# Kernel tuning notes

Measured on AMD Instinct MI355X. Metric: run time of the kernel, lower is better.

## Reference

```python
import jax, jax.numpy as jnp
import numpy as np

B, L, D = 2, 2048, 1024
H = 16
HD = D // H  # 64
WINDOW = 256


def setup_inputs() -> dict:
    key = jax.random.key(0)
    k1, k2, k3 = jax.random.split(key, 3)
    s = 0.02
    return {
        "x": jax.random.normal(k1, (B, L, D), dtype=jnp.float32),
        "w_qkv": jax.random.normal(k2, (D, 3 * D), dtype=jnp.float32) * s,
        "b_qkv": jnp.zeros((3 * D,), dtype=jnp.float32),
        "w_out": jax.random.normal(k3, (D, D), dtype=jnp.float32) * s,
        "b_out": jnp.zeros((D,), dtype=jnp.float32),
    }


def _window_mask(seq_len, window_size, dtype):
    # row i allows cols in [i - w//2, i + w//2] inclusive (symmetric band)
    half = window_size // 2
    i = jnp.arange(seq_len)[:, None]
    j = jnp.arange(seq_len)[None, :]
    allowed = jnp.abs(i - j) <= half
    return jnp.where(allowed, jnp.zeros((), dtype), jnp.asarray(-jnp.inf, dtype))


def reference(x, w_qkv, b_qkv, w_out, b_out):
    b, l, d = x.shape
    qkv = x @ w_qkv + b_qkv                        # [B, L, 3D]
    qkv = qkv.reshape(b, l, 3, H, HD)
    q = jnp.transpose(qkv[:, :, 0], (0, 2, 1, 3))   # [B, H, L, HD]
    k = jnp.transpose(qkv[:, :, 1], (0, 2, 1, 3))
    v = jnp.transpose(qkv[:, :, 2], (0, 2, 1, 3))
    scale = 1.0 / np.sqrt(HD)
    scores = jnp.einsum("bhqd,bhkd->bhqk", q, k) * scale
    scores = scores + _window_mask(l, WINDOW, scores.dtype)[None, None]
    attn = jax.nn.softmax(scores, axis=-1)          # dropout: eval mode (p applied only in training)
    out = jnp.einsum("bhqk,bhkd->bhqd", attn, v)    # [B, H, L, HD]
    out = jnp.transpose(out, (0, 2, 1, 3)).reshape(b, l, d)
    return out @ w_out + b_out
```

## Files before the change

kernel.cpp:

```cpp
#include <hip/hip_runtime.h>
#include <math.h>

#define B_    2
#define L_    2048
#define D_    1024
#define H_    16
#define HD_   64
#define HALF_ 128

typedef __attribute__((ext_vector_type(8))) short short8;
typedef __attribute__((ext_vector_type(4))) float f32x4;

__device__ __forceinline__ unsigned short f2bf(float x) {
  unsigned int u = __float_as_uint(x);
  u = (u + 0x7fffu + ((u >> 16) & 1u)) >> 16;
  return (unsigned short)u;
}

__device__ __forceinline__ void async_cp16(const unsigned short* g, unsigned short* l) {
  __builtin_amdgcn_global_load_lds(
      (const __attribute__((address_space(1))) unsigned int*)g,
      (__attribute__((address_space(3))) unsigned int*)l, 16, 0, 0);
}

__device__ __forceinline__ void tr_round32(const float* __restrict__ in,
                                           unsigned short* __restrict__ hi,
                                           int N, int K, int n0, int k0,
                                           float (*t)[33], int tid) {
  {
    const int kl = tid >> 3, nl = (tid & 7) * 4;
    const float4 v = *(const float4*)&in[(size_t)(k0 + kl) * N + n0 + nl];
    t[kl][nl + 0] = v.x; t[kl][nl + 1] = v.y;
    t[kl][nl + 2] = v.z; t[kl][nl + 3] = v.w;
  }
  __syncthreads();
  {
    const int no = tid >> 3, ko = (tid & 7) * 4;
    ushort4 h;
    h.x = f2bf(t[ko + 0][no]);
    h.y = f2bf(t[ko + 1][no]);
    h.z = f2bf(t[ko + 2][no]);
    h.w = f2bf(t[ko + 3][no]);
    *(ushort4*)&hi[(size_t)(n0 + no) * K + k0 + ko] = h;
  }
}

__global__ __launch_bounds__(256) void prep(const float* __restrict__ x,
                                            unsigned short* __restrict__ x_hi,
                                            const float* __restrict__ w_qkv,
                                            unsigned short* __restrict__ wqkvT,
                                            const float* __restrict__ w_out,
                                            unsigned short* __restrict__ woutT) {
  __shared__ float t[32][33];
  const int bx = blockIdx.x, tid = threadIdx.x;
  if (bx < 4096) {
    const int i = (bx * 256 + tid) * 4;
    const float4 a = *(const float4*)&x[i];
    ushort4 h;
    h.x = f2bf(a.x); h.y = f2bf(a.y); h.z = f2bf(a.z); h.w = f2bf(a.w);
    *(ushort4*)&x_hi[i] = h;
  } else if (bx < 7168) {
    const int tb = bx - 4096;
    tr_round32(w_qkv, wqkvT, 3 * D_, D_, (tb % 96) * 32, (tb / 96) * 32, t, tid);
  } else {
    const int tb = bx - 7168;
    tr_round32(w_out, woutT, D_, D_, (tb % 32) * 32, (tb / 32) * 32, t, tid);
  }
}

__global__ __launch_bounds__(256, 3) void gemm_qkv(
    const unsigned short* __restrict__ Ah,
    const unsigned short* __restrict__ Bh,
    const float* __restrict__ bias,
    unsigned short* __restrict__ q_hi,
    unsigned short* __restrict__ kT,
    unsigned short* __restrict__ vTile,
    int N, int K) {
  __shared__ char smraw[33792];
  const int tid  = threadIdx.x;
  const int wave = tid >> 6, lane = tid & 63;

  const int lin = blockIdx.y * gridDim.x + blockIdx.x;
  const int swz = (lin & 7) * 96 + (lin >> 3);
  const int n0 = (swz % 24) * 128, m0 = (swz / 24) * 128;

  const int wm = (wave >> 1) * 64, wn = (wave & 1) * 64;
  const int quad = lane >> 4, ln16 = lane & 15;

  const bool isA = wave < 2;
  const unsigned short* src = isA ? Ah : Bh;
  const int baserow = isA ? m0 : n0;
  const int instbase = (wave & 1) * 8;
  const int dbase = (isA ? 0 : 16384) + instbase * 1024;
  size_t goff[8];
#pragma unroll
  for (int i = 0; i < 8; ++i) {
    const int r = (instbase + i) * 8 + (lane >> 3);
    const int c = (lane & 7) ^ (r & 7);
    goff[i] = (size_t)(baserow + r) * K + c * 8;
  }

  int offA[4], offB[4];
#pragma unroll
  for (int t = 0; t < 4; ++t) {
    const int r = wm + t * 16 + ln16;
    offA[t] = r * 128 + ((quad ^ (r & 7)) * 16);
    const int rn = wn + t * 16 + ln16;
    offB[t] = 16384 + rn * 128 + ((quad ^ (rn & 7)) * 16);
  }

  f32x4 acc[4][4] = {};
  const char* smb = (const char*)smraw;

  for (int k0 = 0; k0 < K; k0 += 64) {
#pragma unroll
    for (int i = 0; i < 8; ++i)
      async_cp16(src + goff[i] + k0,
                 (unsigned short*)(smraw + dbase + i * 1024));
    __syncthreads();

    {
      short8 ah[4], bh[4];
#pragma unroll
      for (int t = 0; t < 4; ++t) {
        ah[t] = *(const short8*)(smb + offA[t]);
        bh[t] = *(const short8*)(smb + offB[t]);
      }
#pragma unroll
      for (int t = 0; t < 4; ++t)
#pragma unroll
        for (int u = 0; u < 4; ++u)
          acc[t][u] = __builtin_amdgcn_mfma_f32_16x16x32_bf16(bh[u], ah[t], acc[t][u], 0, 0, 0);
    }
    {
      short8 ah[4], bh[4];
#pragma unroll
      for (int t = 0; t < 4; ++t) {
        ah[t] = *(const short8*)(smb + (offA[t] ^ 64));
        bh[t] = *(const short8*)(smb + (offB[t] ^ 64));
      }
#pragma unroll
      for (int t = 0; t < 4; ++t)
#pragma unroll
        for (int u = 0; u < 4; ++u)
          acc[t][u] = __builtin_amdgcn_mfma_f32_16x16x32_bf16(bh[u], ah[t], acc[t][u], 0, 0, 0);
    }
    __syncthreads();
  }

  const int slot = n0 >> 10;
  const int nbase = n0 & 1023;

  if (slot == 0) {
#pragma unroll
    for (int t = 0; t < 4; ++t) {
      const int m = m0 + wm + t * 16 + ln16;
#pragma unroll
      for (int u = 0; u < 4; ++u) {
        const int nl = wn + u * 16 + quad * 4;
        const float4 bq = *(const float4*)&bias[n0 + nl];
        ushort4 h;
        h.x = f2bf(acc[t][u][0] + bq.x);
        h.y = f2bf(acc[t][u][1] + bq.y);
        h.z = f2bf(acc[t][u][2] + bq.z);
        h.w = f2bf(acc[t][u][3] + bq.w);
        *(ushort4*)&q_hi[(size_t)m * 1024 + nbase + nl] = h;
      }
    }
  } else if (slot == 1) {
#pragma unroll
    for (int t = 0; t < 4; ++t) {
      const int tok = m0 + wm + t * 16 + ln16;
      const int bb = tok >> 11, j = tok & 2047;
#pragma unroll
      for (int u = 0; u < 4; ++u) {
        const int nl = wn + u * 16 + quad * 4;
        const float4 bq = *(const float4*)&bias[n0 + nl];
        const int hd = nbase + nl;
        const int hh_ = hd >> 6, dg = (hd & 63) >> 3, di = hd & 7;
        ushort4 h;
        h.x = f2bf(acc[t][u][0] + bq.x);
        h.y = f2bf(acc[t][u][1] + bq.y);
        h.z = f2bf(acc[t][u][2] + bq.z);
        h.w = f2bf(acc[t][u][3] + bq.w);
        const size_t o =
            ((((size_t)bb * 16 + hh_) * 8 + dg) * 2048 + j) * 8 + di;
        *(ushort4*)&kT[o] = h;
      }
    }
  } else {
    unsigned short* lt = (unsigned short*)smraw;
#pragma unroll
    for (int t = 0; t < 4; ++t) {
      const int ml = wm + t * 16 + ln16;
#pragma unroll
      for (int u = 0; u < 4; ++u) {
        const int nl = wn + u * 16 + quad * 4;
        const float4 bq = *(const float4*)&bias[n0 + nl];
        ushort4 h;
        h.x = f2bf(acc[t][u][0] + bq.x);
        h.y = f2bf(acc[t][u][1] + bq.y);
        h.z = f2bf(acc[t][u][2] + bq.z);
        h.w = f2bf(acc[t][u][3] + bq.w);
        *(ushort4*)&lt[ml * 132 + nl] = h;
      }
    }
    __syncthreads();
    const int jg0 = (m0 & 2047) >> 3;
    const int bb = m0 >> 11;
#pragma unroll
    for (int it = 0; it < 8; ++it) {
      const int chunk = it * 256 + tid;
      const int hd = chunk & 127, tokg = chunk >> 7;
      short8 hh;
#pragma unroll
      for (int s = 0; s < 8; ++s)
        hh[s] = (short)lt[(tokg * 8 + s) * 132 + hd];
      const size_t o =
          (((size_t)bb * 256 + jg0 + tokg) * 1024 + nbase + hd) * 8;
      *(short8*)&vTile[o] = hh;
    }
  }
}

__global__ __launch_bounds__(256, 2) void gemm_out(
    const unsigned short* __restrict__ Ah,
    const unsigned short* __restrict__ Bh,
    const float* __restrict__ bias,
    float* __restrict__ C,
    int N, int K) {
  __shared__ char smraw[24576];
  const int tid  = threadIdx.x;
  const int wave = tid >> 6, lane = tid & 63;

  const int lin = blockIdx.y * gridDim.x + blockIdx.x;
  const int swz = (lin & 7) * 64 + (lin >> 3);
  const int n0 = (swz % 16) * 64, m0 = (swz / 16) * 128;

  const int quad = lane >> 4, ln16 = lane & 15;
  const int wm = wave * 32;

  const unsigned short* sptr[6];
  int dstoff[6];
#pragma unroll
  for (int s = 0; s < 6; ++s) {
    const int g = wave * 6 + s;
    const bool isA = g < 16;
    const unsigned short* base = isA ? Ah : Bh;
    const int r0 = isA ? g * 8 : (g - 16) * 8;
    const int r = r0 + (lane >> 3);
    const int c = (lane & 7) ^ (r & 7);
    sptr[s] = base + (size_t)((isA ? m0 : n0) + r) * K + c * 8;
    dstoff[s] = isA ? g * 1024 : 16384 + (g - 16) * 1024;
  }

  int offA[2], offB[4];
#pragma unroll
  for (int t = 0; t < 2; ++t) {
    const int r = wm + t * 16 + ln16;
    offA[t] = r * 128 + ((quad ^ (r & 7)) * 16);
  }
#pragma unroll
  for (int u = 0; u < 4; ++u) {
    const int rn = u * 16 + ln16;
    offB[u] = 16384 + rn * 128 + ((quad ^ (rn & 7)) * 16);
  }

  f32x4 acc[2][4] = {};
  const char* smb = (const char*)smraw;

  for (int k0 = 0; k0 < K; k0 += 64) {
#pragma unroll
    for (int s = 0; s < 6; ++s)
      async_cp16(sptr[s] + k0, (unsigned short*)(smraw + dstoff[s]));
    __syncthreads();

    {
      short8 ah[2], bh[4];
#pragma unroll
      for (int t = 0; t < 2; ++t) ah[t] = *(const short8*)(smb + offA[t]);
#pragma unroll
      for (int u = 0; u < 4; ++u) bh[u] = *(const short8*)(smb + offB[u]);
#pragma unroll
      for (int t = 0; t < 2; ++t)
#pragma unroll
        for (int u = 0; u < 4; ++u)
          acc[t][u] = __builtin_amdgcn_mfma_f32_16x16x32_bf16(bh[u], ah[t], acc[t][u], 0, 0, 0);
    }
    {
      short8 ah[2], bh[4];
#pragma unroll
      for (int t = 0; t < 2; ++t) ah[t] = *(const short8*)(smb + (offA[t] ^ 64));
#pragma unroll
      for (int u = 0; u < 4; ++u) bh[u] = *(const short8*)(smb + (offB[u] ^ 64));
#pragma unroll
      for (int t = 0; t < 2; ++t)
#pragma unroll
        for (int u = 0; u < 4; ++u)
          acc[t][u] = __builtin_amdgcn_mfma_f32_16x16x32_bf16(bh[u], ah[t], acc[t][u], 0, 0, 0);
    }
    __syncthreads();
  }

#pragma unroll
  for (int t = 0; t < 2; ++t) {
    const int m = m0 + wm + t * 16 + ln16;
#pragma unroll
    for (int u = 0; u < 4; ++u) {
      const int n = n0 + u * 16 + quad * 4;
      const float4 bq = *(const float4*)&bias[n];
      float4 o;
      o.x = acc[t][u][0] + bq.x;
      o.y = acc[t][u][1] + bq.y;
      o.z = acc[t][u][2] + bq.z;
      o.w = acc[t][u][3] + bq.w;
      *(float4*)&C[(size_t)m * N + n] = o;
    }
  }
}

__global__ __launch_bounds__(256) void attn_mfma(
    const unsigned short* __restrict__ q_hi,
    const unsigned short* __restrict__ kT,
    const unsigned short* __restrict__ vTile,
    unsigned short* __restrict__ attn_h) {
  __shared__ float ob[64 * 68];

  const int tid = threadIdx.x;
  const int mt  = tid >> 6, lane = tid & 63;
  const int quad = lane >> 4, ln16 = lane & 15;

  const int lin  = blockIdx.x + gridDim.x * (blockIdx.y + gridDim.y * blockIdx.z);
  const int xcd  = lin & 7, idx = lin >> 3;
  const int pair = xcd * 4 + (idx >> 5);
  const int i0   = (idx & 31) * 64;
  const int b    = pair >> 4, h = pair & 15;
  const int jlo  = i0 - HALF_;

  const size_t qbase =
      (size_t)(b * L_ + i0 + mt * 16 + ln16) * 1024 + h * 64 + quad * 8;
  const short8 qh0 = *(const short8*)&q_hi[qbase];
  const short8 qh1 = *(const short8*)&q_hi[qbase + 32];

  const size_t kb0 = (((size_t)b * 16 + h) * 8 + quad) * 2048 * 8;
  const size_t kb1 = (((size_t)b * 16 + h) * 8 + quad + 4) * 2048 * 8;

  const int iabs = i0 + mt * 16 + ln16;

  f32x4 o[4] = {};
  float s = 0.f;

  short8 kf[2][4], vf[2][4];
  {
    const int base = jlo;
    const int j0c = min(max(base + ln16, 0), L_ - 1);
    const int j1c = min(max(base + 16 + ln16, 0), L_ - 1);
    kf[0][0] = *(const short8*)&kT[kb0 + (size_t)j0c * 8];
    kf[0][1] = *(const short8*)&kT[kb1 + (size_t)j0c * 8];
    kf[0][2] = *(const short8*)&kT[kb0 + (size_t)j1c * 8];
    kf[0][3] = *(const short8*)&kT[kb1 + (size_t)j1c * 8];
    const int jv = min(max(base + quad * 8, 0), L_ - 8);
    const size_t vgb = ((size_t)b * 256 + (jv >> 3)) * 1024 + h * 64;
#pragma unroll
    for (int t = 0; t < 4; ++t)
      vf[0][t] = *(const short8*)&vTile[(vgb + t * 16 + ln16) * 8];
  }

#pragma unroll
  for (int c = 0; c < 10; ++c) {
    const int cur = c & 1, nxt = cur ^ 1;

    if (c < 9) {
      const int nb = jlo + (c + 1) * 32;
      const int j0c = min(max(nb + ln16, 0), L_ - 1);
      const int j1c = min(max(nb + 16 + ln16, 0), L_ - 1);
      kf[nxt][0] = *(const short8*)&kT[kb0 + (size_t)j0c * 8];
      kf[nxt][1] = *(const short8*)&kT[kb1 + (size_t)j0c * 8];
      kf[nxt][2] = *(const short8*)&kT[kb0 + (size_t)j1c * 8];
      kf[nxt][3] = *(const short8*)&kT[kb1 + (size_t)j1c * 8];
      const int jv = min(max(nb + quad * 8, 0), L_ - 8);
      const size_t vgb = ((size_t)b * 256 + (jv >> 3)) * 1024 + h * 64;
#pragma unroll
      for (int t = 0; t < 4; ++t)
        vf[nxt][t] = *(const short8*)&vTile[(vgb + t * 16 + ln16) * 8];
    }

    const int base = jlo + c * 32;

    f32x4 a0 = {}, a1 = {};
    __builtin_amdgcn_s_setprio(1);
    a0 = __builtin_amdgcn_mfma_f32_16x16x32_bf16(kf[cur][0], qh0, a0, 0, 0, 0);
    a0 = __builtin_amdgcn_mfma_f32_16x16x32_bf16(kf[cur][1], qh1, a0, 0, 0, 0);
    a1 = __builtin_amdgcn_mfma_f32_16x16x32_bf16(kf[cur][2], qh0, a1, 0, 0, 0);
    a1 = __builtin_amdgcn_mfma_f32_16x16x32_bf16(kf[cur][3], qh1, a1, 0, 0, 0);
    __builtin_amdgcn_s_setprio(0);

    unsigned int pk00, pk01, pk10, pk11;
    {
      float ev[4];
#pragma unroll
      for (int e = 0; e < 4; ++e) {
        const int jabs = base + quad * 4 + e;
        const bool ok = (jabs >= 0) && (jabs < L_) && (abs(iabs - jabs) <= HALF_);
        ev[e] = ok ? __expf(a0[e] * 0.125f) : 0.f;
        s += ev[e];
      }
      pk00 = (unsigned)f2bf(ev[0]) | ((unsigned)f2bf(ev[1]) << 16);
      pk01 = (unsigned)f2bf(ev[2]) | ((unsigned)f2bf(ev[3]) << 16);
    }
    {
      float ev[4];
#pragma unroll
      for (int e = 0; e < 4; ++e) {
        const int jabs = base + 16 + quad * 4 + e;
        const bool ok = (jabs >= 0) && (jabs < L_) && (abs(iabs - jabs) <= HALF_);
        ev[e] = ok ? __expf(a1[e] * 0.125f) : 0.f;
        s += ev[e];
      }
      pk10 = (unsigned)f2bf(ev[0]) | ((unsigned)f2bf(ev[1]) << 16);
      pk11 = (unsigned)f2bf(ev[2]) | ((unsigned)f2bf(ev[3]) << 16);
    }

    const int src0 = ((quad & 1) * 2) * 16 + ln16;
    const int src1 = src0 + 16;
    const unsigned a0w = (unsigned)__shfl((int)pk00, src0);
    const unsigned b0w = (unsigned)__shfl((int)pk10, src0);
    const unsigned a1w = (unsigned)__shfl((int)pk01, src0);
    const unsigned b1w = (unsigned)__shfl((int)pk11, src0);
    const unsigned a2w = (unsigned)__shfl((int)pk00, src1);
    const unsigned b2w = (unsigned)__shfl((int)pk10, src1);
    const unsigned a3w = (unsigned)__shfl((int)pk01, src1);
    const unsigned b3w = (unsigned)__shfl((int)pk11, src1);
    int4 wv;
    wv.x = (int)((quad < 2) ? a0w : b0w);
    wv.y = (int)((quad < 2) ? a1w : b1w);
    wv.z = (int)((quad < 2) ? a2w : b2w);
    wv.w = (int)((quad < 2) ? a3w : b3w);
    const short8 pf = *(const short8*)&wv;

    __builtin_amdgcn_s_setprio(1);
#pragma unroll
    for (int t = 0; t < 4; ++t)
      o[t] = __builtin_amdgcn_mfma_f32_16x16x32_bf16(pf, vf[cur][t], o[t], 0, 0, 0);
    __builtin_amdgcn_s_setprio(0);
  }

  s += __shfl_xor(s, 16);
  s += __shfl_xor(s, 32);
  float rinv[4];
#pragma unroll
  for (int e = 0; e < 4; ++e)
    rinv[e] = 1.f / __shfl(s, quad * 4 + e);

#pragma unroll
  for (int t = 0; t < 4; ++t)
#pragma unroll
    for (int e = 0; e < 4; ++e)
      ob[(mt * 16 + quad * 4 + e) * 68 + t * 16 + ln16] = o[t][e] * rinv[e];
  __syncthreads();
#pragma unroll
  for (int pass = 0; pass < 2; ++pass) {
    const int rr = pass * 32 + (tid >> 3), ck = tid & 7;
    const float* rp = &ob[rr * 68 + ck * 8];
    const float4 f0 = *(const float4*)&rp[0];
    const float4 f1 = *(const float4*)&rp[4];
    short8 hh;
    hh[0] = (short)f2bf(f0.x); hh[1] = (short)f2bf(f0.y);
    hh[2] = (short)f2bf(f0.z); hh[3] = (short)f2bf(f0.w);
    hh[4] = (short)f2bf(f1.x); hh[5] = (short)f2bf(f1.y);
    hh[6] = (short)f2bf(f1.z); hh[7] = (short)f2bf(f1.w);
    const size_t oo = ((size_t)(b * L_ + i0 + rr)) * 1024 + h * 64 + ck * 8;
    *(short8*)&attn_h[oo] = hh;
  }
}

extern "C" void kernel_launch(void* const* d_in, const int* in_sizes, int n_in,
                              void* d_out, int out_size, void* d_ws, size_t ws_size,
                              hipStream_t stream) {
  const float* x     = (const float*)d_in[0];
  const float* w_qkv = (const float*)d_in[1];
  const float* b_qkv = (const float*)d_in[2];
  const float* w_out = (const float*)d_in[3];
  const float* b_out = (const float*)d_in[4];
  float* out = (float*)d_out;

  const int M = B_ * L_;

  char* ws = (char*)d_ws;
  unsigned short* x_hi    = (unsigned short*)(ws + 0);
  unsigned short* wqkvT   = (unsigned short*)(ws + 16777216);
  unsigned short* woutT   = (unsigned short*)(ws + 23068672);
  unsigned short* q_hi    = (unsigned short*)(ws + 25165824);
  unsigned short* kT      = (unsigned short*)(ws + 33554432);
  unsigned short* vTile   = (unsigned short*)(ws + 41943040);
  unsigned short* attn_hi = (unsigned short*)(ws + 0);

  prep<<<8192, 256, 0, stream>>>(x, x_hi, w_qkv, wqkvT, w_out, woutT);
  {
    dim3 g(3072 / 128, M / 128);
    gemm_qkv<<<g, 256, 0, stream>>>(x_hi, wqkvT, b_qkv, q_hi, kT, vTile,
                                    3072, D_);
  }
  {
    dim3 g(L_ / 64, H_, B_);
    attn_mfma<<<g, 256, 0, stream>>>(q_hi, kT, vTile, attn_hi);
  }
  {
    dim3 g(D_ / 64, M / 128);
    gemm_out<<<g, 256, 0, stream>>>(attn_hi, woutT, b_out, out, D_, D_);
  }
}
```

Measured before the change: 155.9 us.

## Double-buffer LDS staging in QKV and output GEMMs with K-step 32

Both bf16 GEMMs switch from a single LDS buffer with K-step 64 to two LDS buffers with K-step 32. The next tile's async global-to-LDS copy is issued before the MFMAs on the current tile, so load latency can overlap with compute. The loader mapping and the XOR swizzle are rebuilt for 64-byte rows. In exchange there are twice as many loop iterations and barriers, each with fewer MFMAs per wait. Every iteration ends with a full vmcnt(0) wait, which limits how much overlap is possible.

New measurement: 157.3 us. About the same (+0.9%).

```diff
diff --git a/kernel.cpp b/kernel.cpp
--- a/kernel.cpp
+++ b/kernel.cpp
@@ -87,66 +87,63 @@
   const int wm = (wave >> 1) * 64, wn = (wave & 1) * 64;
   const int quad = lane >> 4, ln16 = lane & 15;
 
-  const bool isA = wave < 2;
-  const unsigned short* src = isA ? Ah : Bh;
-  const int baserow = isA ? m0 : n0;
-  const int instbase = (wave & 1) * 8;
-  const int dbase = (isA ? 0 : 16384) + instbase * 1024;
-  size_t goff[8];
-#pragma unroll
-  for (int i = 0; i < 8; ++i) {
-    const int r = (instbase + i) * 8 + (lane >> 3);
-    const int c = (lane & 7) ^ (r & 7);
-    goff[i] = (size_t)(baserow + r) * K + c * 8;
+  const int srow   = tid >> 2;
+  const int schunk = tid & 3;
+  size_t gsrc[4];
+  int doff[4];
+#pragma unroll
+  for (int s = 0; s < 4; ++s) {
+    const bool isA = s < 2;
+    const int r = (s & 1) * 64 + srow;
+    const int c = schunk ^ ((r >> 1) & 3);
+    gsrc[s] = (size_t)((isA ? m0 : n0) + r) * K + c * 8;
+    doff[s] = (isA ? 0 : 8192) + (s & 1) * 4096 + wave * 1024;
+  }
+
+#define STAGE_QKV(bufoff, ko)                                                   \
+  {                                                                             \
+    async_cp16(Ah + gsrc[0] + (ko), (unsigned short*)(smraw + (bufoff) + doff[0])); \
+    async_cp16(Ah + gsrc[1] + (ko), (unsigned short*)(smraw + (bufoff) + doff[1])); \
+    async_cp16(Bh + gsrc[2] + (ko), (unsigned short*)(smraw + (bufoff) + doff[2])); \
+    async_cp16(Bh + gsrc[3] + (ko), (unsigned short*)(smraw + (bufoff) + doff[3])); \
   }
 
   int offA[4], offB[4];
 #pragma unroll
   for (int t = 0; t < 4; ++t) {
     const int r = wm + t * 16 + ln16;
-    offA[t] = r * 128 + ((quad ^ (r & 7)) * 16);
+    offA[t] = r * 64 + ((quad ^ ((r >> 1) & 3)) * 16);
     const int rn = wn + t * 16 + ln16;
-    offB[t] = 16384 + rn * 128 + ((quad ^ (rn & 7)) * 16);
+    offB[t] = 8192 + rn * 64 + ((quad ^ ((rn >> 1) & 3)) * 16);
   }
 
   f32x4 acc[4][4] = {};
-  const char* smb = (const char*)smraw;
-
-  for (int k0 = 0; k0 < K; k0 += 64) {
-#pragma unroll
-    for (int i = 0; i < 8; ++i)
-      async_cp16(src + goff[i] + k0,
-                 (unsigned short*)(smraw + dbase + i * 1024));
-    __syncthreads();
-
-    {
-      short8 ah[4], bh[4];
-#pragma unroll
-      for (int t = 0; t < 4; ++t) {
-        ah[t] = *(const short8*)(smb + offA[t]);
-        bh[t] = *(const short8*)(smb + offB[t]);
-      }
-#pragma unroll
-      for (int t = 0; t < 4; ++t)
-#pragma unroll
-        for (int u = 0; u < 4; ++u)
-          acc[t][u] = __builtin_amdgcn_mfma_f32_16x16x32_bf16(bh[u], ah[t], acc[t][u], 0, 0, 0);
-    }
-    {
-      short8 ah[4], bh[4];
-#pragma unroll
-      for (int t = 0; t < 4; ++t) {
-        ah[t] = *(const short8*)(smb + (offA[t] ^ 64));
-        bh[t] = *(const short8*)(smb + (offB[t] ^ 64));
-      }
-#pragma unroll
-      for (int t = 0; t < 4; ++t)
-#pragma unroll
-        for (int u = 0; u < 4; ++u)
-          acc[t][u] = __builtin_amdgcn_mfma_f32_16x16x32_bf16(bh[u], ah[t], acc[t][u], 0, 0, 0);
-    }
-    __syncthreads();
-  }
+
+  STAGE_QKV(0, 0);
+  asm volatile("s_waitcnt vmcnt(0)" ::: "memory");
+  __builtin_amdgcn_s_barrier();
+
+  for (int kt = 0; kt < 32; ++kt) {
+    const int cur = (kt & 1) * 16384;
+    if (kt < 31) STAGE_QKV(16384 - cur, (kt + 1) * 32);
+
+    const char* buf = smraw + cur;
+    short8 ah[4], bh[4];
+#pragma unroll
+    for (int t = 0; t < 4; ++t) {
+      ah[t] = *(const short8*)(buf + offA[t]);
+      bh[t] = *(const short8*)(buf + offB[t]);
+    }
+#pragma unroll
+    for (int t = 0; t < 4; ++t)
+#pragma unroll
+      for (int u = 0; u < 4; ++u)
+        acc[t][u] = __builtin_amdgcn_mfma_f32_16x16x32_bf16(bh[u], ah[t], acc[t][u], 0, 0, 0);
+
+    asm volatile("s_waitcnt vmcnt(0)" ::: "memory");
+    __builtin_amdgcn_s_barrier();
+  }
+#undef STAGE_QKV
 
   const int slot = n0 >> 10;
   const int nbase = n0 & 1023;
@@ -240,67 +237,64 @@
   const int quad = lane >> 4, ln16 = lane & 15;
   const int wm = wave * 32;
 
-  const unsigned short* sptr[6];
-  int dstoff[6];
-#pragma unroll
-  for (int s = 0; s < 6; ++s) {
-    const int g = wave * 6 + s;
-    const bool isA = g < 16;
-    const unsigned short* base = isA ? Ah : Bh;
-    const int r0 = isA ? g * 8 : (g - 16) * 8;
-    const int r = r0 + (lane >> 3);
-    const int c = (lane & 7) ^ (r & 7);
-    sptr[s] = base + (size_t)((isA ? m0 : n0) + r) * K + c * 8;
-    dstoff[s] = isA ? g * 1024 : 16384 + (g - 16) * 1024;
+  const int srow   = tid >> 2;
+  const int schunk = tid & 3;
+  size_t gsrc[3];
+  int doff[3];
+#pragma unroll
+  for (int s = 0; s < 3; ++s) {
+    const bool isA = s < 2;
+    const int r = (isA ? (s & 1) * 64 : 0) + srow;
+    const int c = schunk ^ ((r >> 1) & 3);
+    gsrc[s] = (size_t)((isA ? m0 : n0) + r) * K + c * 8;
+    doff[s] = (isA ? (s & 1) * 4096 : 8192) + wave * 1024;
+  }
+
+#define STAGE_OUT(bufoff, ko)                                                   \
+  {                                                                             \
+    async_cp16(Ah + gsrc[0] + (ko), (unsigned short*)(smraw + (bufoff) + doff[0])); \
+    async_cp16(Ah + gsrc[1] + (ko), (unsigned short*)(smraw + (bufoff) + doff[1])); \
+    async_cp16(Bh + gsrc[2] + (ko), (unsigned short*)(smraw + (bufoff) + doff[2])); \
   }
 
   int offA[2], offB[4];
 #pragma unroll
   for (int t = 0; t < 2; ++t) {
     const int r = wm + t * 16 + ln16;
-    offA[t] = r * 128 + ((quad ^ (r & 7)) * 16);
+    offA[t] = r * 64 + ((quad ^ ((r >> 1) & 3)) * 16);
   }
 #pragma unroll
   for (int u = 0; u < 4; ++u) {
     const int rn = u * 16 + ln16;
-    offB[u] = 16384 + rn * 128 + ((quad ^ (rn & 7)) * 16);
+    offB[u] = 8192 + rn * 64 + ((quad ^ ((rn >> 1) & 3)) * 16);
   }
 
   f32x4 acc[2][4] = {};
-  const char* smb = (const char*)smraw;
-
-  for (int k0 = 0; k0 < K; k0 += 64) {
-#pragma unroll
-    for (int s = 0; s < 6; ++s)
-      async_cp16(sptr[s] + k0, (unsigned short*)(smraw + dstoff[s]));
-    __syncthreads();
-
-    {
-      short8 ah[2], bh[4];
-#pragma unroll
-      for (int t = 0; t < 2; ++t) ah[t] = *(const short8*)(smb + offA[t]);
-#pragma unroll
-      for (int u = 0; u < 4; ++u) bh[u] = *(const short8*)(smb + offB[u]);
-#pragma unroll
-      for (int t = 0; t < 2; ++t)
-#pragma unroll
-        for (int u = 0; u < 4; ++u)
-          acc[t][u] = __builtin_amdgcn_mfma_f32_16x16x32_bf16(bh[u], ah[t], acc[t][u], 0, 0, 0);
-    }
-    {
-      short8 ah[2], bh[4];
-#pragma unroll
-      for (int t = 0; t < 2; ++t) ah[t] = *(const short8*)(smb + (offA[t] ^ 64));
-#pragma unroll
-      for (int u = 0; u < 4; ++u) bh[u] = *(const short8*)(smb + (offB[u] ^ 64));
-#pragma unroll
-      for (int t = 0; t < 2; ++t)
-#pragma unroll
-        for (int u = 0; u < 4; ++u)
-          acc[t][u] = __builtin_amdgcn_mfma_f32_16x16x32_bf16(bh[u], ah[t], acc[t][u], 0, 0, 0);
-    }
-    __syncthreads();
-  }
+
+  STAGE_OUT(0, 0);
+  asm volatile("s_waitcnt vmcnt(0)" ::: "memory");
+  __builtin_amdgcn_s_barrier();
+
+  for (int kt = 0; kt < 32; ++kt) {
+    const int cur = (kt & 1) * 12288;
+    if (kt < 31) STAGE_OUT(12288 - cur, (kt + 1) * 32);
+
+    const char* buf = smraw + cur;
+    short8 ah[2], bh[4];
+#pragma unroll
+    for (int t = 0; t < 2; ++t) ah[t] = *(const short8*)(buf + offA[t]);
+#pragma unroll
+    for (int u = 0; u < 4; ++u) bh[u] = *(const short8*)(buf + offB[u]);
+#pragma unroll
+    for (int t = 0; t < 2; ++t)
+#pragma unroll
+      for (int u = 0; u < 4; ++u)
+        acc[t][u] = __builtin_amdgcn_mfma_f32_16x16x32_bf16(bh[u], ah[t], acc[t][u], 0, 0, 0);
+
+    asm volatile("s_waitcnt vmcnt(0)" ::: "memory");
+    __builtin_amdgcn_s_barrier();
+  }
+#undef STAGE_OUT
 
 #pragma unroll
   for (int t = 0; t < 2; ++t) {
```
